# Kernel optimization log

Hardware: AMD Instinct MI355X
Metric: run time of the kernel (lower is better)

Reference implementation:

```python
import jax, jax.numpy as jnp
import numpy as np

N, D, R = 65536, 32, 128


def setup_inputs() -> dict:
    key = jax.random.key(0)
    k1, k2, k3, k4 = jax.random.split(key, 4)
    X = jax.random.normal(k1, (N, D), dtype=jnp.float32)
    a = jax.random.normal(k2, (R, D), dtype=jnp.float32)
    b = jax.random.uniform(k3, (R, D), dtype=jnp.float32)  # positive, like abs(randn)
    c = jax.random.normal(k4, (R, D + 1), dtype=jnp.float32)
    return {"X": X, "a": a, "b": b, "c": c}


def reference(X, a, b, c):
    # Gaussian membership per (sample, rule, dim): exp(-(x-a)^2 / (2*clamp(b,1e-8)^2))
    b_cl = jnp.clip(b, 1e-8)                      # [R, D]
    diff = X[:, None, :] - a[None, :, :]          # [N, R, D]
    mu = jnp.exp(-(diff * diff) / (2.0 * b_cl * b_cl))
    strengths = jnp.prod(mu, axis=2)              # [N, R] rule firing strengths
    strengths_sum = jnp.sum(strengths, axis=1, keepdims=True)
    normalized = strengths / (strengths_sum + 1e-8)
    # consequent: linear model per rule, X @ c[:, :-1].T + bias
    rule_out = X @ c[:, :-1].T + c[:, -1]         # [N, R]
    predictions = jnp.sum(normalized * rule_out, axis=1)  # [N]
    return (predictions, strengths, normalized)
```

## Files before the change

### kernel.cpp

```cpp
#include <hip/hip_runtime.h>

#define NS 65536
#define DD 32
#define RR 128
#define SPB 16
#define STR 132

__global__ __launch_bounds__(128, 3) void anfis_main(
    const float* __restrict__ X, const float* __restrict__ A,
    const float* __restrict__ B, const float* __restrict__ C,
    float* __restrict__ out_pred, float* __restrict__ out_str,
    float* __restrict__ out_norm)
{
    __shared__ float SBUF[SPB * STR];
    __shared__ float PBUF[SPB * STR];
    __shared__ float XT[SPB * DD];
    __shared__ float pS[SPB][8];
    __shared__ float pD[SPB][8];
    __shared__ float scale_lds[SPB];

    const int tid   = threadIdx.x;
    const int nbase = blockIdx.x * SPB;

    ((float4*)XT)[tid] = ((const float4*)(X + (size_t)nbase * DD))[tid];

    float w_[DD], naw_[DD], ck_[DD], bias;
    {
        const float4* av = (const float4*)(A + tid * DD);
        const float4* bv = (const float4*)(B + tid * DD);
        #pragma unroll
        for (int i = 0; i < 8; ++i) {
            float4 va = av[i], vb = bv[i];
            float w0 = 0.8493218003f * __builtin_amdgcn_rcpf(fmaxf(vb.x, 1e-8f));
            float w1 = 0.8493218003f * __builtin_amdgcn_rcpf(fmaxf(vb.y, 1e-8f));
            float w2 = 0.8493218003f * __builtin_amdgcn_rcpf(fmaxf(vb.z, 1e-8f));
            float w3 = 0.8493218003f * __builtin_amdgcn_rcpf(fmaxf(vb.w, 1e-8f));
            w_[4*i+0] = w0; naw_[4*i+0] = -va.x * w0;
            w_[4*i+1] = w1; naw_[4*i+1] = -va.y * w1;
            w_[4*i+2] = w2; naw_[4*i+2] = -va.z * w2;
            w_[4*i+3] = w3; naw_[4*i+3] = -va.w * w3;
        }
        #pragma unroll
        for (int d = 0; d < DD; ++d) ck_[d] = C[tid * (DD + 1) + d];
        bias = C[tid * (DD + 1) + DD];
    }
    __syncthreads();

    #pragma unroll
    for (int d = 0; d < DD; ++d)
        asm("" : "+v"(w_[d]), "+v"(naw_[d]), "+v"(ck_[d]));
    asm("" : "+v"(bias));

    #define LOADH(buf, jj, hh) { _Pragma("unroll") \
        for (int g = 0; g < 4; ++g) \
            buf[g] = *(const float4*)&XT[(jj) * DD + (hh) * 16 + g * 4]; }

    #define COMPUTEH(buf, d0) { _Pragma("unroll") \
        for (int g = 0; g < 4; ++g) { \
            const int d = (d0) + g * 4; \
            float4 v = buf[g]; \
            float t0 = fmaf(v.x, w_[d+0], naw_[d+0]); s0 = fmaf(t0, t0, s0); r0 = fmaf(v.x, ck_[d+0], r0); \
            float t1 = fmaf(v.y, w_[d+1], naw_[d+1]); s1 = fmaf(t1, t1, s1); r1 = fmaf(v.y, ck_[d+1], r1); \
            float t2 = fmaf(v.z, w_[d+2], naw_[d+2]); s2 = fmaf(t2, t2, s2); r2 = fmaf(v.z, ck_[d+2], r2); \
            float t3 = fmaf(v.w, w_[d+3], naw_[d+3]); s3 = fmaf(t3, t3, s3); r3 = fmaf(v.w, ck_[d+3], r3); \
        } }

    float4 qa[4], qb[4];
    LOADH(qa, 0, 0)
    #pragma unroll 2
    for (int j = 0; j < SPB; ++j) {
        float s0 = 0.f, s1 = 0.f, s2 = 0.f, s3 = 0.f;
        float r0 = bias, r1 = 0.f, r2 = 0.f, r3 = 0.f;
        LOADH(qb, j, 1)
        COMPUTEH(qa, 0)
        LOADH(qa, (j + 1) & (SPB - 1), 0)
        COMPUTEH(qb, 16)
        float st = __builtin_amdgcn_exp2f(-((s0 + s1) + (s2 + s3)));
        float ro = (r0 + r1) + (r2 + r3);
        SBUF[j * STR + tid] = st;
        PBUF[j * STR + tid] = st * ro;
    }
    #undef LOADH
    #undef COMPUTEH
    __syncthreads();

    {
        int s = tid >> 3, o = tid & 7;
        const float4* srow = (const float4*)&SBUF[s * STR + o * 16];
        const float4* prow = (const float4*)&PBUF[s * STR + o * 16];
        float ss = 0.f, dd = 0.f;
        #pragma unroll
        for (int k = 0; k < 4; ++k) {
            float4 v = srow[k]; ss += (v.x + v.y) + (v.z + v.w);
            float4 p = prow[k]; dd += (p.x + p.y) + (p.z + p.w);
        }
        pS[s][o] = ss; pD[s][o] = dd;
    }
    __syncthreads();
    if (tid < SPB) {
        float ss = 0.f, dd = 0.f;
        #pragma unroll
        for (int o = 0; o < 8; ++o) { ss += pS[tid][o]; dd += pD[tid][o]; }
        float sc = 1.0f / (ss + 1e-8f);
        out_pred[nbase + tid] = dd * sc;
        scale_lds[tid] = sc;
    }
    __syncthreads();

    #pragma unroll
    for (int it = 0; it < 4; ++it) {
        int f   = it * 128 + tid;
        int row = f >> 5;
        int col = f & 31;
        float4 v = *(const float4*)&SBUF[row * STR + col * 4];
        float sc = scale_lds[row];
        size_t base = ((size_t)(nbase + row)) * RR + col * 4;
        *(float4*)(out_str  + base) = v;
        *(float4*)(out_norm + base) = make_float4(v.x * sc, v.y * sc, v.z * sc, v.w * sc);
    }
}

extern "C" void kernel_launch(void* const* d_in, const int* in_sizes, int n_in,
                              void* d_out, int out_size, void* d_ws, size_t ws_size,
                              hipStream_t stream) {
    const float* X = (const float*)d_in[0];
    const float* A = (const float*)d_in[1];
    const float* B = (const float*)d_in[2];
    const float* C = (const float*)d_in[3];

    float* pred = (float*)d_out;
    float* str  = pred + NS;
    float* nrm  = str + (size_t)NS * RR;

    anfis_main<<<dim3(NS / SPB), dim3(128), 0, stream>>>(X, A, B, C, pred, str, nrm);
}
```

Baseline: 107.9 us.

## Process two sample tiles per block and prefetch the second X tile

Each block now handles two 16-sample tiles (grid halved to 2048 blocks), so the per-rule parameters (w, a, c) loaded into registers are reused across both tiles. The X data for the second tile is fetched into registers before the first tile's compute and stored to a second LDS buffer afterwards, hiding its load latency. The cost is an extra barrier between tiles and fewer blocks, which lowers parallelism and the ability to overlap stores across blocks.

Result: no change. 109.1 us (+1.1%).

```diff
diff --git a/kernel.cpp b/kernel.cpp
--- a/kernel.cpp
+++ b/kernel.cpp
@@ -5,6 +5,7 @@
 #define RR 128
 #define SPB 16
 #define STR 132
+#define NBLK 2048
 
 __global__ __launch_bounds__(128, 3) void anfis_main(
     const float* __restrict__ X, const float* __restrict__ A,
@@ -14,15 +15,16 @@
 {
     __shared__ float SBUF[SPB * STR];
     __shared__ float PBUF[SPB * STR];
-    __shared__ float XT[SPB * DD];
+    __shared__ float XT[2][SPB * DD];
     __shared__ float pS[SPB][8];
     __shared__ float pD[SPB][8];
     __shared__ float scale_lds[SPB];
 
-    const int tid   = threadIdx.x;
-    const int nbase = blockIdx.x * SPB;
+    const int tid = threadIdx.x;
+    const int t0  = blockIdx.x;
+    const int t1  = blockIdx.x + NBLK;
 
-    ((float4*)XT)[tid] = ((const float4*)(X + (size_t)nbase * DD))[tid];
+    ((float4*)XT[0])[tid] = ((const float4*)(X + (size_t)t0 * SPB * DD))[tid];
 
     float w_[DD], naw_[DD], ck_[DD], bias;
     {
@@ -51,73 +53,85 @@
         asm("" : "+v"(w_[d]), "+v"(naw_[d]), "+v"(ck_[d]));
     asm("" : "+v"(bias));
 
-    #define LOADH(buf, jj, hh) { _Pragma("unroll") \
+    float4 px = ((const float4*)(X + (size_t)t1 * SPB * DD))[tid];
+
+    #define LOADH(xt, buf, jj, hh) { _Pragma("unroll") \
         for (int g = 0; g < 4; ++g) \
-            buf[g] = *(const float4*)&XT[(jj) * DD + (hh) * 16 + g * 4]; }
+            buf[g] = *(const float4*)&(xt)[(jj) * DD + (hh) * 16 + g * 4]; }
 
     #define COMPUTEH(buf, d0) { _Pragma("unroll") \
         for (int g = 0; g < 4; ++g) { \
             const int d = (d0) + g * 4; \
             float4 v = buf[g]; \
-            float t0 = fmaf(v.x, w_[d+0], naw_[d+0]); s0 = fmaf(t0, t0, s0); r0 = fmaf(v.x, ck_[d+0], r0); \
-            float t1 = fmaf(v.y, w_[d+1], naw_[d+1]); s1 = fmaf(t1, t1, s1); r1 = fmaf(v.y, ck_[d+1], r1); \
-            float t2 = fmaf(v.z, w_[d+2], naw_[d+2]); s2 = fmaf(t2, t2, s2); r2 = fmaf(v.z, ck_[d+2], r2); \
-            float t3 = fmaf(v.w, w_[d+3], naw_[d+3]); s3 = fmaf(t3, t3, s3); r3 = fmaf(v.w, ck_[d+3], r3); \
+            float t0_ = fmaf(v.x, w_[d+0], naw_[d+0]); s0 = fmaf(t0_, t0_, s0); r0 = fmaf(v.x, ck_[d+0], r0); \
+            float t1_ = fmaf(v.y, w_[d+1], naw_[d+1]); s1 = fmaf(t1_, t1_, s1); r1 = fmaf(v.y, ck_[d+1], r1); \
+            float t2_ = fmaf(v.z, w_[d+2], naw_[d+2]); s2 = fmaf(t2_, t2_, s2); r2 = fmaf(v.z, ck_[d+2], r2); \
+            float t3_ = fmaf(v.w, w_[d+3], naw_[d+3]); s3 = fmaf(t3_, t3_, s3); r3 = fmaf(v.w, ck_[d+3], r3); \
         } }
 
-    float4 qa[4], qb[4];
-    LOADH(qa, 0, 0)
-    #pragma unroll 2
-    for (int j = 0; j < SPB; ++j) {
-        float s0 = 0.f, s1 = 0.f, s2 = 0.f, s3 = 0.f;
-        float r0 = bias, r1 = 0.f, r2 = 0.f, r3 = 0.f;
-        LOADH(qb, j, 1)
-        COMPUTEH(qa, 0)
-        LOADH(qa, (j + 1) & (SPB - 1), 0)
-        COMPUTEH(qb, 16)
-        float st = __builtin_amdgcn_exp2f(-((s0 + s1) + (s2 + s3)));
-        float ro = (r0 + r1) + (r2 + r3);
-        SBUF[j * STR + tid] = st;
-        PBUF[j * STR + tid] = st * ro;
+    for (int tt = 0; tt < 2; ++tt) {
+        const int   nbase = (tt ? t1 : t0) * SPB;
+        const float* xt   = XT[tt];
+
+        float4 qa[4], qb[4];
+        LOADH(xt, qa, 0, 0)
+        #pragma unroll 2
+        for (int j = 0; j < SPB; ++j) {
+            float s0 = 0.f, s1 = 0.f, s2 = 0.f, s3 = 0.f;
+            float r0 = bias, r1 = 0.f, r2 = 0.f, r3 = 0.f;
+            LOADH(xt, qb, j, 1)
+            COMPUTEH(qa, 0)
+            LOADH(xt, qa, (j + 1) & (SPB - 1), 0)
+            COMPUTEH(qb, 16)
+            float st = __builtin_amdgcn_exp2f(-((s0 + s1) + (s2 + s3)));
+            float ro = (r0 + r1) + (r2 + r3);
+            SBUF[j * STR + tid] = st;
+            PBUF[j * STR + tid] = st * ro;
+        }
+        __syncthreads();
+
+        {
+            int s = tid >> 3, o = tid & 7;
+            const float4* srow = (const float4*)&SBUF[s * STR + o * 16];
+            const float4* prow = (const float4*)&PBUF[s * STR + o * 16];
+            float ss = 0.f, dd = 0.f;
+            #pragma unroll
+            for (int k = 0; k < 4; ++k) {
+                float4 v = srow[k]; ss += (v.x + v.y) + (v.z + v.w);
+                float4 p = prow[k]; dd += (p.x + p.y) + (p.z + p.w);
+            }
+            pS[s][o] = ss; pD[s][o] = dd;
+        }
+        __syncthreads();
+        if (tid < SPB) {
+            float ss = 0.f, dd = 0.f;
+            #pragma unroll
+            for (int o = 0; o < 8; ++o) { ss += pS[tid][o]; dd += pD[tid][o]; }
+            float sc = 1.0f / (ss + 1e-8f);
+            out_pred[nbase + tid] = dd * sc;
+            scale_lds[tid] = sc;
+        }
+        __syncthreads();
+
+        #pragma unroll
+        for (int it = 0; it < 4; ++it) {
+            int f   = it * 128 + tid;
+            int row = f >> 5;
+            int col = f & 31;
+            float4 v = *(const float4*)&SBUF[row * STR + col * 4];
+            float sc = scale_lds[row];
+            size_t base = ((size_t)(nbase + row)) * RR + col * 4;
+            *(float4*)(out_str  + base) = v;
+            *(float4*)(out_norm + base) = make_float4(v.x * sc, v.y * sc, v.z * sc, v.w * sc);
+        }
+
+        if (tt == 0) {
+            ((float4*)XT[1])[tid] = px;
+            __syncthreads();
+        }
     }
     #undef LOADH
     #undef COMPUTEH
-    __syncthreads();
-
-    {
-        int s = tid >> 3, o = tid & 7;
-        const float4* srow = (const float4*)&SBUF[s * STR + o * 16];
-        const float4* prow = (const float4*)&PBUF[s * STR + o * 16];
-        float ss = 0.f, dd = 0.f;
-        #pragma unroll
-        for (int k = 0; k < 4; ++k) {
-            float4 v = srow[k]; ss += (v.x + v.y) + (v.z + v.w);
-            float4 p = prow[k]; dd += (p.x + p.y) + (p.z + p.w);
-        }
-        pS[s][o] = ss; pD[s][o] = dd;
-    }
-    __syncthreads();
-    if (tid < SPB) {
-        float ss = 0.f, dd = 0.f;
-        #pragma unroll
-        for (int o = 0; o < 8; ++o) { ss += pS[tid][o]; dd += pD[tid][o]; }
-        float sc = 1.0f / (ss + 1e-8f);
-        out_pred[nbase + tid] = dd * sc;
-        scale_lds[tid] = sc;
-    }
-    __syncthreads();
-
-    #pragma unroll
-    for (int it = 0; it < 4; ++it) {
-        int f   = it * 128 + tid;
-        int row = f >> 5;
-        int col = f & 31;
-        float4 v = *(const float4*)&SBUF[row * STR + col * 4];
-        float sc = scale_lds[row];
-        size_t base = ((size_t)(nbase + row)) * RR + col * 4;
-        *(float4*)(out_str  + base) = v;
-        *(float4*)(out_norm + base) = make_float4(v.x * sc, v.y * sc, v.z * sc, v.w * sc);
-    }
 }
 
 extern "C" void kernel_launch(void* const* d_in, const int* in_sizes, int n_in,
@@ -132,5 +146,5 @@
     float* str  = pred + NS;
     float* nrm  = str + (size_t)NS * RR;
 
-    anfis_main<<<dim3(NS / SPB), dim3(128), 0, stream>>>(X, A, B, C, pred, str, nrm);
+    anfis_main<<<dim3(NBLK), dim3(128), 0, stream>>>(X, A, B, C, pred, str, nrm);
 }
```
